# Kernel tuning notes

Measured on AMD Instinct MI355X. Metric: run time of the kernel, lower is better.

## Reference

```python
import jax, jax.numpy as jnp
import numpy as np

B, S, D = 32, 512, 512
H, DH = 8, 64          # head_num, att_embedding_size
DFF = 4 * D
NEG = float(-2**32 + 1)
LN_EPS = 1e-3          # keras LayerNormalization default


def layer_norm(x, gamma, beta):
    mu = jnp.mean(x, axis=-1, keepdims=True)
    var = jnp.mean(jnp.square(x - mu), axis=-1, keepdims=True)
    return (x - mu) / jnp.sqrt(var + LN_EPS) * gamma + beta


def setup_inputs() -> dict:
    key = jax.random.key(0)
    ks = jax.random.split(key, 10)
    queries = jax.random.normal(ks[0], (B, S, D), dtype=jnp.float32)
    keys = jax.random.normal(ks[1], (B, S, D), dtype=jnp.float32)
    query_lens = jax.random.randint(ks[2], (B, 1), 1, S + 1)
    key_lens = jax.random.randint(ks[3], (B, 1), 1, S + 1)
    # learned params (TruncatedNormal stddev 0.05-ish / Glorot approximated by scaled normals)
    W_Q = jax.random.normal(ks[4], (D, D), dtype=jnp.float32) * 0.05
    W_K = jax.random.normal(ks[5], (D, D), dtype=jnp.float32) * 0.05
    W_V = jax.random.normal(ks[6], (D, D), dtype=jnp.float32) * 0.05
    fw1 = jax.random.normal(ks[7], (D, DFF), dtype=jnp.float32) * (1.0 / np.sqrt(D))
    fw2 = jax.random.normal(ks[8], (DFF, D), dtype=jnp.float32) * (1.0 / np.sqrt(DFF))
    ln_gamma = jnp.ones((D,), dtype=jnp.float32)
    ln_beta = jnp.zeros((D,), dtype=jnp.float32)
    return {"queries": queries, "keys": keys, "W_Q": W_Q, "W_K": W_K, "W_V": W_V,
            "fw1": fw1, "fw2": fw2, "ln_gamma": ln_gamma, "ln_beta": ln_beta,
            "query_lens": query_lens, "key_lens": key_lens}


def reference(queries, keys, W_Q, W_K, W_V, fw1, fw2, ln_gamma, ln_beta, query_lens, key_lens):
    # masks from sequence lengths: [B, S] float {0,1}
    pos = jnp.arange(S)
    q_mask = (pos[None, :] < query_lens).astype(queries.dtype)  # [B,S]
    k_mask = (pos[None, :] < key_lens).astype(queries.dtype)    # [B,S]

    # QKV projections, split into heads: [B,S,H,DH]
    Q = (queries @ W_Q).reshape(B, S, H, DH)
    Kp = (keys @ W_K).reshape(B, S, H, DH)
    V = (keys @ W_V).reshape(B, S, H, DH)

    # scaled dot-product scores: [B,H,Sq,Sk]
    scores = jnp.einsum('bqhd,bkhd->bhqk', Q, Kp) / jnp.sqrt(jnp.asarray(DH, queries.dtype))

    # key padding mask
    scores = jnp.where(k_mask[:, None, None, :] == 1, scores, NEG)
    # blinding: kill the diagonal (self-position)
    eye = jnp.eye(S, dtype=bool)
    scores = jnp.where(eye[None, None, :, :], NEG, scores)

    scores = scores - jnp.max(scores, axis=-1, keepdims=True)
    attn = jax.nn.softmax(scores, axis=-1)
    # query mask zeros out padded query rows (after softmax, as in source)
    attn = attn * q_mask[:, None, :, None]

    out = jnp.einsum('bhqk,bkhd->bqhd', attn, V).reshape(B, S, D)

    result = out + queries                       # use_res
    result = layer_norm(result, ln_gamma, ln_beta)  # shared ln (use_layer_norm)

    # feed-forward
    h = jax.nn.relu(result @ fw1) @ fw2
    result = result + h
    result = layer_norm(result, ln_gamma, ln_beta)

    # output_type == 'mean'
    return jnp.mean(result, axis=1, keepdims=True)  # [B,1,D]
```

## Files before the change

kernel.cpp:

```cpp
#include <hip/hip_runtime.h>

typedef unsigned short ushort_t;
typedef unsigned int uint_t;
typedef __attribute__((ext_vector_type(4))) float f32x4;
typedef __attribute__((ext_vector_type(2))) float f32x2;
typedef __attribute__((ext_vector_type(8))) short s16x8;
typedef __attribute__((ext_vector_type(8))) _Float16 f16x8;
typedef __attribute__((ext_vector_type(4))) unsigned short u16x4;

#define NEGV -60000.0f

__device__ __forceinline__ ushort_t f2bf(float f) {
  unsigned int u = __builtin_bit_cast(unsigned int, f);
  return (ushort_t)((u + 0x7fffu + ((u >> 16) & 1u)) >> 16);
}
__device__ __forceinline__ float bf2f(ushort_t h) {
  unsigned int u = ((unsigned int)h) << 16;
  return __builtin_bit_cast(float, u);
}
__device__ __forceinline__ void gload_lds16(const void* g, void* l) {
  __builtin_amdgcn_global_load_lds(
      (const __attribute__((address_space(1))) unsigned int*)g,
      (__attribute__((address_space(3))) unsigned int*)l, 16, 0, 0);
}

template<int EPI>
__global__ __launch_bounds__(512, 2)
void gemm256(const ushort_t* __restrict__ A, const ushort_t* __restrict__ A2,
             int lda,
             const ushort_t* __restrict__ Bt, int ldb,
             void* __restrict__ Cv, int ldc, int K,
             long long sB, long long sC)
{
  __shared__ ushort_t Asm[2][16384];
  __shared__ ushort_t Bsm[2][16384];

  const int tid = threadIdx.x, wid = tid >> 6, lane = tid & 63;
  const int wr = wid >> 2, wc = wid & 3;
  const int fr = lane & 15, fq = lane >> 4;
  const int z = blockIdx.z;

  const ushort_t* Az = (z == 0) ? A : A2;
  const ushort_t* Bz = Bt + (size_t)z * sB;

  const int orig = blockIdx.x + gridDim.x * blockIdx.y;
  const int bx = (orig >> 3) % gridDim.x;
  const int by = (orig & 7) + 8 * ((orig >> 3) / gridDim.x);
  const int m0 = by * 256, n0 = bx * 256;

  const int rr0 = tid >> 3;
  const int ks = (((tid & 7) ^ (rr0 & 7)) * 8);

  auto stageA = [&](int p, int kt, int h) {
    const ushort_t* s = Az + (size_t)(m0 + h * 128 + rr0) * lda + kt * 64 + ks;
    ushort_t* d = &Asm[p][h * 8192 + tid * 8];
    gload_lds16(s, d);
    gload_lds16(s + (size_t)64 * lda, d + 4096);
  };
  auto stageB = [&](int p, int kt, int h) {
    const ushort_t* s = Bz + (size_t)(n0 + h * 128 + rr0) * ldb + kt * 64 + ks;
    ushort_t* d = &Bsm[p][h * 8192 + tid * 8];
    gload_lds16(s, d);
    gload_lds16(s + (size_t)64 * ldb, d + 4096);
  };
  auto ldA = [&](int p, int mi, int kc) -> s16x8 {
    const int R = wr * 128 + mi * 16 + fr;
    return *(const s16x8*)(&Asm[p][R * 64 + (((kc * 4 + fq) ^ (fr & 7)) * 8)]);
  };
  auto ldB = [&](int p, int ni, int kc) -> s16x8 {
    const int R = wc * 64 + ni * 16 + fr;
    return *(const s16x8*)(&Bsm[p][R * 64 + (((kc * 4 + fq) ^ (fr & 7)) * 8)]);
  };

  f32x4 acc[8][4];
#pragma unroll
  for (int m = 0; m < 8; ++m)
#pragma unroll
    for (int n = 0; n < 4; ++n)
      acc[m][n] = (f32x4){0.f, 0.f, 0.f, 0.f};

  const int nk = K >> 6;
  const int niter = nk >> 1;

  stageB(0, 0, 0); stageB(0, 0, 1);
  stageA(0, 0, 0); stageA(0, 0, 1);
  stageB(1, 1, 0); stageB(1, 1, 1);
  asm volatile("s_waitcnt vmcnt(4)" ::: "memory");
  __builtin_amdgcn_s_barrier();

  s16x8 af[4][2], bf[4][2];

  for (int it = 0; it < niter; ++it) {
    const int T = 2 * it;
    const bool more = (it + 1 < niter);

#pragma unroll
    for (int mi = 0; mi < 4; ++mi)
#pragma unroll
      for (int kc = 0; kc < 2; ++kc) af[mi][kc] = ldA(0, mi, kc);
#pragma unroll
    for (int ni = 0; ni < 2; ++ni)
#pragma unroll
      for (int kc = 0; kc < 2; ++kc) bf[ni][kc] = ldB(0, ni, kc);
    stageA(1, T + 1, 0);
    __builtin_amdgcn_s_barrier();
    asm volatile("s_waitcnt lgkmcnt(0)" ::: "memory");
    __builtin_amdgcn_s_setprio(1);
#pragma unroll
    for (int mi = 0; mi < 4; ++mi)
#pragma unroll
      for (int ni = 0; ni < 2; ++ni)
#pragma unroll
        for (int kc = 0; kc < 2; ++kc)
          acc[mi][ni] = __builtin_amdgcn_mfma_f32_16x16x32_bf16(
              af[mi][kc], bf[ni][kc], acc[mi][ni], 0, 0, 0);
    __builtin_amdgcn_s_setprio(0);
    __builtin_amdgcn_s_barrier();

#pragma unroll
    for (int ni = 2; ni < 4; ++ni)
#pragma unroll
      for (int kc = 0; kc < 2; ++kc) bf[ni][kc] = ldB(0, ni, kc);
    stageA(1, T + 1, 1);
    __builtin_amdgcn_s_barrier();
    asm volatile("s_waitcnt lgkmcnt(0)" ::: "memory");
    __builtin_amdgcn_s_setprio(1);
#pragma unroll
    for (int mi = 0; mi < 4; ++mi)
#pragma unroll
      for (int ni = 2; ni < 4; ++ni)
#pragma unroll
        for (int kc = 0; kc < 2; ++kc)
          acc[mi][ni] = __builtin_amdgcn_mfma_f32_16x16x32_bf16(
              af[mi][kc], bf[ni][kc], acc[mi][ni], 0, 0, 0);
    __builtin_amdgcn_s_setprio(0);
    __builtin_amdgcn_s_barrier();

#pragma unroll
    for (int mi = 0; mi < 4; ++mi)
#pragma unroll
      for (int kc = 0; kc < 2; ++kc) af[mi][kc] = ldA(0, 4 + mi, kc);
    if (more) stageB(0, T + 2, 0);
    __builtin_amdgcn_s_barrier();
    asm volatile("s_waitcnt lgkmcnt(0)" ::: "memory");
    __builtin_amdgcn_s_setprio(1);
#pragma unroll
    for (int mi = 0; mi < 4; ++mi)
#pragma unroll
      for (int ni = 0; ni < 2; ++ni)
#pragma unroll
        for (int kc = 0; kc < 2; ++kc)
          acc[4 + mi][ni] = __builtin_amdgcn_mfma_f32_16x16x32_bf16(
              af[mi][kc], bf[ni][kc], acc[4 + mi][ni], 0, 0, 0);
    __builtin_amdgcn_s_setprio(0);
    __builtin_amdgcn_s_barrier();

    if (more) {
      stageB(0, T + 2, 1);
      asm volatile("s_waitcnt vmcnt(4)" ::: "memory");
    } else {
      asm volatile("s_waitcnt vmcnt(0)" ::: "memory");
    }
    __builtin_amdgcn_s_barrier();
    __builtin_amdgcn_s_setprio(1);
#pragma unroll
    for (int mi = 0; mi < 4; ++mi)
#pragma unroll
      for (int ni = 2; ni < 4; ++ni)
#pragma unroll
        for (int kc = 0; kc < 2; ++kc)
          acc[4 + mi][ni] = __builtin_amdgcn_mfma_f32_16x16x32_bf16(
              af[mi][kc], bf[ni][kc], acc[4 + mi][ni], 0, 0, 0);
    __builtin_amdgcn_s_setprio(0);
    __builtin_amdgcn_s_barrier();

#pragma unroll
    for (int mi = 0; mi < 4; ++mi)
#pragma unroll
      for (int kc = 0; kc < 2; ++kc) af[mi][kc] = ldA(1, mi, kc);
#pragma unroll
    for (int ni = 0; ni < 2; ++ni)
#pragma unroll
      for (int kc = 0; kc < 2; ++kc) bf[ni][kc] = ldB(1, ni, kc);
    if (more) stageA(0, T + 2, 0);
    __builtin_amdgcn_s_barrier();
    asm volatile("s_waitcnt lgkmcnt(0)" ::: "memory");
    __builtin_amdgcn_s_setprio(1);
#pragma unroll
    for (int mi = 0; mi < 4; ++mi)
#pragma unroll
      for (int ni = 0; ni < 2; ++ni)
#pragma unroll
        for (int kc = 0; kc < 2; ++kc)
          acc[mi][ni] = __builtin_amdgcn_mfma_f32_16x16x32_bf16(
              af[mi][kc], bf[ni][kc], acc[mi][ni], 0, 0, 0);
    __builtin_amdgcn_s_setprio(0);
    __builtin_amdgcn_s_barrier();

#pragma unroll
    for (int ni = 2; ni < 4; ++ni)
#pragma unroll
      for (int kc = 0; kc < 2; ++kc) bf[ni][kc] = ldB(1, ni, kc);
    if (more) stageA(0, T + 2, 1);
    __builtin_amdgcn_s_barrier();
    asm volatile("s_waitcnt lgkmcnt(0)" ::: "memory");
    __builtin_amdgcn_s_setprio(1);
#pragma unroll
    for (int mi = 0; mi < 4; ++mi)
#pragma unroll
      for (int ni = 2; ni < 4; ++ni)
#pragma unroll
        for (int kc = 0; kc < 2; ++kc)
          acc[mi][ni] = __builtin_amdgcn_mfma_f32_16x16x32_bf16(
              af[mi][kc], bf[ni][kc], acc[mi][ni], 0, 0, 0);
    __builtin_amdgcn_s_setprio(0);
    __builtin_amdgcn_s_barrier();

#pragma unroll
    for (int mi = 0; mi < 4; ++mi)
#pragma unroll
      for (int kc = 0; kc < 2; ++kc) af[mi][kc] = ldA(1, 4 + mi, kc);
    if (more) stageB(1, T + 3, 0);
    __builtin_amdgcn_s_barrier();
    asm volatile("s_waitcnt lgkmcnt(0)" ::: "memory");
    __builtin_amdgcn_s_setprio(1);
#pragma unroll
    for (int mi = 0; mi < 4; ++mi)
#pragma unroll
      for (int ni = 0; ni < 2; ++ni)
#pragma unroll
        for (int kc = 0; kc < 2; ++kc)
          acc[4 + mi][ni] = __builtin_amdgcn_mfma_f32_16x16x32_bf16(
              af[mi][kc], bf[ni][kc], acc[4 + mi][ni], 0, 0, 0);
    __builtin_amdgcn_s_setprio(0);
    __builtin_amdgcn_s_barrier();

    if (more) {
      stageB(1, T + 3, 1);
      asm volatile("s_waitcnt vmcnt(4)" ::: "memory");
    } else {
      asm volatile("s_waitcnt vmcnt(0)" ::: "memory");
    }
    __builtin_amdgcn_s_barrier();
    __builtin_amdgcn_s_setprio(1);
#pragma unroll
    for (int mi = 0; mi < 4; ++mi)
#pragma unroll
      for (int ni = 2; ni < 4; ++ni)
#pragma unroll
        for (int kc = 0; kc < 2; ++kc)
          acc[4 + mi][ni] = __builtin_amdgcn_mfma_f32_16x16x32_bf16(
              af[mi][kc], bf[ni][kc], acc[4 + mi][ni], 0, 0, 0);
    __builtin_amdgcn_s_setprio(0);
    __builtin_amdgcn_s_barrier();
  }

  const float s0 = (EPI == 4 && z == 0) ? 0.125f : 1.0f;
  char* Cz = (char*)Cv + (size_t)sC * z;
  const int rb = fq * 4;
#pragma unroll
  for (int mi = 0; mi < 8; ++mi)
#pragma unroll
    for (int ni = 0; ni < 4; ++ni)
#pragma unroll
      for (int j = 0; j < 4; ++j) {
        const int rg = m0 + wr * 128 + mi * 16 + rb + j;
        const int cg = n0 + wc * 64 + ni * 16 + fr;
        float v = acc[mi][ni][j];
        const size_t idx = (size_t)rg * ldc + cg;
        if constexpr (EPI == 0) {
          ((float*)Cz)[idx] = v;
        } else if constexpr (EPI == 2) {
          ((ushort_t*)Cz)[idx] = f2bf(fmaxf(v, 0.f));
        } else {
          ((ushort_t*)Cz)[idx] = f2bf(v * s0);
        }
      }
}

__global__ __launch_bounds__(256, 4)
void flash_attn(const ushort_t* __restrict__ Qg, const ushort_t* __restrict__ Kg,
                const ushort_t* __restrict__ Vt, ushort_t* __restrict__ AOb,
                const int* __restrict__ qlen, const int* __restrict__ klen)
{
  __shared__ ushort_t sm[20480];
  ushort_t* PQ = sm + 16384;

  const int tid = threadIdx.x, w = tid >> 6, lane = tid & 63;
  const int fr = lane & 15, fq = lane >> 4;

  int id = blockIdx.x;
  id = (id & 7) * 256 + (id >> 3);
  const int qt = id & 7, h = (id >> 3) & 7, b = id >> 6;
  const int q0 = qt * 64;
  const int KL = klen[b], QL = qlen[b];

  if (q0 >= QL) {
#pragma unroll
    for (int i = 0; i < 4; ++i) {
      int idx = i * 256 + tid;
      int rr = idx >> 4, cc = (idx & 15) << 2;
      *(u16x4*)&AOb[((size_t)(b * 512 + q0 + rr)) * 512 + h * 64 + cc] =
          (u16x4){0, 0, 0, 0};
    }
    return;
  }

  int nt = (KL + 63) >> 6;
  if (KL == 1) nt = 8;

  const ushort_t* Qrow = Qg + ((size_t)(b * 512 + q0)) * 512 + h * 64;
  const ushort_t* Krow = Kg + ((size_t)b * 512) * 512 + h * 64;
  const ushort_t* Vrow = Vt + (((size_t)b * 8 + h) * 64) * 512;

#pragma unroll
  for (int i = 0; i < 2; ++i) {
    int s = i * 256 + tid, r = s >> 3, c = (s & 7) ^ (r & 7);
    gload_lds16(Qrow + (size_t)r * 512 + c * 8, PQ + (i * 256 + w * 64) * 8);
  }
#pragma unroll
  for (int i = 0; i < 2; ++i) {
    int s = i * 256 + tid, r = s >> 3, c = (s & 7) ^ (r & 7);
    gload_lds16(Krow + (size_t)r * 512 + c * 8, sm + (i * 256 + w * 64) * 8);
    gload_lds16(Vrow + (size_t)r * 512 + c * 8, sm + 4096 + (i * 256 + w * 64) * 8);
  }
  __syncthreads();

  s16x8 qf[2];
#pragma unroll
  for (int kc = 0; kc < 2; ++kc) {
    int r = w * 16 + fr;
    qf[kc] = *(const s16x8*)(PQ + r * 64 + (((kc * 4 + fq) ^ (r & 7)) * 8));
  }

  float mrun[4], lrun[4];
  f32x4 oacc[4];
#pragma unroll
  for (int j = 0; j < 4; ++j) { mrun[j] = -1e30f; lrun[j] = 0.f; }
#pragma unroll
  for (int nd = 0; nd < 4; ++nd) oacc[nd] = (f32x4){0.f, 0.f, 0.f, 0.f};

  for (int t = 0; t < nt; ++t) {
    ushort_t* Kb = sm + (t & 1) * 8192;
    ushort_t* Vb = Kb + 4096;
    if (t + 1 < nt) {
      const int kv1 = (t + 1) * 64;
      ushort_t* Kn = sm + ((t + 1) & 1) * 8192;
#pragma unroll
      for (int i = 0; i < 2; ++i) {
        int s = i * 256 + tid, r = s >> 3, c = (s & 7) ^ (r & 7);
        gload_lds16(Krow + (size_t)(kv1 + r) * 512 + c * 8,
                    Kn + (i * 256 + w * 64) * 8);
        gload_lds16(Vrow + (size_t)r * 512 + kv1 + c * 8,
                    Kn + 4096 + (i * 256 + w * 64) * 8);
      }
    }
    const int kv0 = t * 64;

    f32x4 sacc[4];
#pragma unroll
    for (int n = 0; n < 4; ++n) sacc[n] = (f32x4){0.f, 0.f, 0.f, 0.f};
#pragma unroll
    for (int n = 0; n < 4; ++n)
#pragma unroll
      for (int kc = 0; kc < 2; ++kc) {
        int r = n * 16 + fr;
        s16x8 kf = *(const s16x8*)(Kb + r * 64 + (((kc * 4 + fq) ^ (r & 7)) * 8));
        sacc[n] = __builtin_amdgcn_mfma_f32_16x16x32_bf16(qf[kc], kf, sacc[n], 0, 0, 0);
      }

#pragma unroll
    for (int j = 0; j < 4; ++j) {
      const int rl = w * 16 + fq * 4 + j;
      const int rg = q0 + rl;
      float sv[4];
      float tmax = -1e30f;
#pragma unroll
      for (int n = 0; n < 4; ++n) {
        int cg = kv0 + n * 16 + fr;
        float v = sacc[n][j];
        if (cg >= KL || cg == rg) v = NEGV;
        sv[n] = v;
        tmax = fmaxf(tmax, v);
      }
#pragma unroll
      for (int o = 1; o < 16; o <<= 1) tmax = fmaxf(tmax, __shfl_xor(tmax, o));
      const float mnew = fmaxf(mrun[j], tmax);
      const float sf = __expf(mrun[j] - mnew);
      mrun[j] = mnew;
      float ps = 0.f;
      _Float16* prow = (_Float16*)(PQ + rl * 64);
#pragma unroll
      for (int n = 0; n < 4; ++n) {
        float p = __expf(sv[n] - mnew);
        ps += p;
        int cl = n * 2 + (fr >> 3);
        prow[((cl ^ (rl & 7)) * 8) + (fr & 7)] = (_Float16)p;
      }
      lrun[j] = lrun[j] * sf + ps;
#pragma unroll
      for (int nd = 0; nd < 4; ++nd) oacc[nd][j] *= sf;
    }

#pragma unroll
    for (int kc = 0; kc < 2; ++kc) {
      const int rl = w * 16 + fr;
      s16x8 pf = *(const s16x8*)(PQ + rl * 64 + (((kc * 4 + fq) ^ (rl & 7)) * 8));
#pragma unroll
      for (int nd = 0; nd < 4; ++nd) {
        int d = nd * 16 + fr;
        s16x8 vf = *(const s16x8*)(Vb + d * 64 + (((kc * 4 + fq) ^ (d & 7)) * 8));
        oacc[nd] = __builtin_amdgcn_mfma_f32_16x16x32_f16(
            __builtin_bit_cast(f16x8, pf), __builtin_bit_cast(f16x8, vf),
            oacc[nd], 0, 0, 0);
      }
    }
    __syncthreads();
  }

#pragma unroll
  for (int j = 0; j < 4; ++j) {
    float l = lrun[j];
#pragma unroll
    for (int o = 1; o < 16; o <<= 1) l += __shfl_xor(l, o);
    const int rg = q0 + w * 16 + fq * 4 + j;
    const float inv = (rg < QL) ? (1.f / l) : 0.f;
#pragma unroll
    for (int nd = 0; nd < 4; ++nd)
      AOb[((size_t)(b * 512 + rg)) * 512 + h * 64 + nd * 16 + fr] =
          f2bf(oacc[nd][j] * inv);
  }
}

__global__ __launch_bounds__(256) void cvt_bf16(const float* __restrict__ in,
                                                ushort_t* __restrict__ out, int n4) {
  int i = blockIdx.x * 256 + threadIdx.x;
  if (i >= n4) return;
  f32x4 v = ((const f32x4*)in)[i];
  u16x4 o;
#pragma unroll
  for (int j = 0; j < 4; ++j) o[j] = f2bf(v[j]);
  ((u16x4*)out)[i] = o;
}

__global__ __launch_bounds__(256) void transpose_cvt(const float* __restrict__ in,
                                                     ushort_t* __restrict__ out,
                                                     int R, int C) {
  __shared__ float tile[32][33];
  const int c0 = blockIdx.x * 32, r0 = blockIdx.y * 32;
  const int tx = threadIdx.x & 31, ty = threadIdx.x >> 5;
#pragma unroll
  for (int i = 0; i < 32; i += 8)
    tile[ty + i][tx] = in[(size_t)(r0 + ty + i) * C + (c0 + tx)];
  __syncthreads();
#pragma unroll
  for (int i = 0; i < 32; i += 8)
    out[(size_t)(c0 + ty + i) * R + (r0 + tx)] = f2bf(tile[tx][ty + i]);
}

__global__ __launch_bounds__(256) void build_vt(const ushort_t* __restrict__ V,
                                                ushort_t* __restrict__ Vt) {
  __shared__ ushort_t tile[64 * 65];
  const int s0 = blockIdx.x * 64, h = blockIdx.y, b = blockIdx.z;
  const int t = threadIdx.x;
#pragma unroll
  for (int i = 0; i < 16; ++i) {
    int idx = i * 256 + t;
    int sl = idx >> 6, d = idx & 63;
    tile[sl * 65 + d] = V[(size_t)(b * 512 + s0 + sl) * 512 + h * 64 + d];
  }
  __syncthreads();
  _Float16* vt = (_Float16*)Vt;
#pragma unroll
  for (int i = 0; i < 16; ++i) {
    int idx = i * 256 + t;
    int d = idx >> 6, sl = idx & 63;
    vt[((size_t)(b * 8 + h) * 64 + d) * 512 + (s0 + sl)] =
        (_Float16)bf2f(tile[sl * 65 + d]);
  }
}

__global__ __launch_bounds__(256) void ln1(const ushort_t* __restrict__ xb,
                                           const float* __restrict__ r,
                                           const float* __restrict__ g,
                                           const float* __restrict__ be,
                                           ushort_t* __restrict__ ob) {
  const int row = blockIdx.x, t = threadIdx.x;
  const size_t base = (size_t)row * 512;
  const uint_t xv = ((const uint_t*)(xb + base))[t];
  const f32x2 rv = ((const f32x2*)(r + base))[t];
  float v0 = bf2f((ushort_t)(xv & 0xffff)) + rv[0];
  float v1 = bf2f((ushort_t)(xv >> 16)) + rv[1];
  float s = v0 + v1, q = v0 * v0 + v1 * v1;
#pragma unroll
  for (int o = 32; o; o >>= 1) { s += __shfl_xor(s, o); q += __shfl_xor(q, o); }
  __shared__ float ps[4], pq[4];
  const int w = t >> 6, lane = t & 63;
  if (lane == 0) { ps[w] = s; pq[w] = q; }
  __syncthreads();
  s = ps[0] + ps[1] + ps[2] + ps[3];
  q = pq[0] + pq[1] + pq[2] + pq[3];
  const float mu = s * 0.001953125f;
  const float var = q * 0.001953125f - mu * mu;
  const float inv = 1.0f / sqrtf(var + 1e-3f);
  const float y0 = (v0 - mu) * inv * g[2 * t] + be[2 * t];
  const float y1 = (v1 - mu) * inv * g[2 * t + 1] + be[2 * t + 1];
  ((uint_t*)(ob + base))[t] = (uint_t)f2bf(y0) | ((uint_t)f2bf(y1) << 16);
}

__global__ __launch_bounds__(256) void ln2(const float* __restrict__ h2a,
                                           const float* __restrict__ h2b,
                                           const ushort_t* __restrict__ r1b,
                                           const float* __restrict__ g,
                                           const float* __restrict__ be,
                                           ushort_t* __restrict__ ob) {
  const int row = blockIdx.x, t = threadIdx.x;
  const size_t base = (size_t)row * 512;
  const f32x2 a = ((const f32x2*)(h2a + base))[t];
  const f32x2 b = ((const f32x2*)(h2b + base))[t];
  const uint_t rv = ((const uint_t*)(r1b + base))[t];
  float v0 = a[0] + b[0] + bf2f((ushort_t)(rv & 0xffff));
  float v1 = a[1] + b[1] + bf2f((ushort_t)(rv >> 16));
  float s = v0 + v1, q = v0 * v0 + v1 * v1;
#pragma unroll
  for (int o = 32; o; o >>= 1) { s += __shfl_xor(s, o); q += __shfl_xor(q, o); }
  __shared__ float ps[4], pq[4];
  const int w = t >> 6, lane = t & 63;
  if (lane == 0) { ps[w] = s; pq[w] = q; }
  __syncthreads();
  s = ps[0] + ps[1] + ps[2] + ps[3];
  q = pq[0] + pq[1] + pq[2] + pq[3];
  const float mu = s * 0.001953125f;
  const float var = q * 0.001953125f - mu * mu;
  const float inv = 1.0f / sqrtf(var + 1e-3f);
  const float y0 = (v0 - mu) * inv * g[2 * t] + be[2 * t];
  const float y1 = (v1 - mu) * inv * g[2 * t + 1] + be[2 * t + 1];
  ((uint_t*)(ob + base))[t] = (uint_t)f2bf(y0) | ((uint_t)f2bf(y1) << 16);
}

__global__ void mean_partial(const ushort_t* __restrict__ r3,
                             float* __restrict__ part) {
  const int sc = blockIdx.x, b = blockIdx.y, d = threadIdx.x;
  float s = 0.f;
#pragma unroll 4
  for (int i = 0; i < 64; ++i)
    s += bf2f(r3[(size_t)(b * 512 + sc * 64 + i) * 512 + d]);
  part[(size_t)(b * 8 + sc) * 512 + d] = s;
}
__global__ void mean_final(const float* __restrict__ part, float* __restrict__ out) {
  const int b = blockIdx.x, d = threadIdx.x;
  float s = 0.f;
#pragma unroll
  for (int i = 0; i < 8; ++i) s += part[(size_t)(b * 8 + i) * 512 + d];
  out[b * 512 + d] = s * (1.0f / 512.0f);
}

extern "C" void kernel_launch(void* const* d_in, const int* in_sizes, int n_in,
                              void* d_out, int out_size, void* d_ws, size_t ws_size,
                              hipStream_t stream) {
  (void)in_sizes; (void)n_in; (void)out_size; (void)ws_size;
  const float* queries = (const float*)d_in[0];
  const float* keys    = (const float*)d_in[1];
  const float* W_Q = (const float*)d_in[2];
  const float* W_K = (const float*)d_in[3];
  const float* W_V = (const float*)d_in[4];
  const float* fw1 = (const float*)d_in[5];
  const float* fw2 = (const float*)d_in[6];
  const float* ln_g = (const float*)d_in[7];
  const float* ln_b = (const float*)d_in[8];
  const int* qlen = (const int*)d_in[9];
  const int* klen = (const int*)d_in[10];
  float* out = (float*)d_out;

  char* ws = (char*)d_ws;
  const size_t MB = 1048576;
  ushort_t* XQ  = (ushort_t*)(ws + 0 * MB);
  ushort_t* XK  = (ushort_t*)(ws + 16 * MB);
  ushort_t* Qb  = (ushort_t*)(ws + 32 * MB);
  ushort_t* Vb  = (ushort_t*)(ws + 64 * MB);
  ushort_t* VT  = (ushort_t*)(ws + 80 * MB);
  ushort_t* AOb = (ushort_t*)(ws + 96 * MB);
  ushort_t* R1B = (ushort_t*)(ws + 112 * MB);
  ushort_t* H1  = (ushort_t*)(ws + 0 * MB);
  float*    H2  = (float*)(ws + 128 * MB);
  ushort_t* R3B = (ushort_t*)(ws + 192 * MB);
  char*     wsw = ws + 208 * MB;
  ushort_t* WQT  = (ushort_t*)(wsw);
  ushort_t* FW1T = (ushort_t*)(wsw + 3 * 524288);
  ushort_t* FW2T = (ushort_t*)(wsw + 3 * 524288 + 2097152);
  float*    PART = (float*)(wsw + 3 * 524288 + 2 * 2097152);

  cvt_bf16<<<8192, 256, 0, stream>>>(queries, XQ, 2097152);
  cvt_bf16<<<8192, 256, 0, stream>>>(keys, XK, 2097152);
  transpose_cvt<<<dim3(16, 16), 256, 0, stream>>>(W_Q, WQT, 512, 512);
  transpose_cvt<<<dim3(16, 16), 256, 0, stream>>>(W_K, WQT + 262144, 512, 512);
  transpose_cvt<<<dim3(16, 16), 256, 0, stream>>>(W_V, WQT + 524288, 512, 512);
  transpose_cvt<<<dim3(64, 16), 256, 0, stream>>>(fw1, FW1T, 512, 2048);
  transpose_cvt<<<dim3(16, 64), 256, 0, stream>>>(fw2, FW2T, 2048, 512);
  gemm256<4><<<dim3(2, 64, 3), 512, 0, stream>>>(
      XQ, XK, 512, WQT, 512, (void*)Qb, 512, 512, 262144, 16 * MB);
  build_vt<<<dim3(8, 8, 32), 256, 0, stream>>>(Vb, VT);
  flash_attn<<<2048, 256, 0, stream>>>(Qb, Qb + 8388608, VT, AOb, qlen, klen);
  ln1<<<16384, 256, 0, stream>>>(AOb, queries, ln_g, ln_b, R1B);
  gemm256<2><<<dim3(8, 64, 1), 512, 0, stream>>>(
      R1B, R1B, 512, FW1T, 512, (void*)H1, 2048, 512, 0, 0);
  gemm256<0><<<dim3(2, 64, 2), 512, 0, stream>>>(
      H1, H1 + 1024, 2048, FW2T, 2048, (void*)H2, 512, 1024, 1024, 32 * MB);
  ln2<<<16384, 256, 0, stream>>>(H2, H2 + 8388608, R1B, ln_g, ln_b, R3B);
  mean_partial<<<dim3(8, 32), 512, 0, stream>>>(R3B, PART);
  mean_final<<<32, 512, 0, stream>>>(PART, out);
}
```

Baseline: 247.3 us.

## Restructure GEMM main loop into four phases and merge prep kernels

The GEMM inner loop drops from eight half-width MFMA phases with a barrier each to four full-width phases. Whole A/B half-tiles are now staged in pairs with adjusted vmcnt waits, and the prologue also prefetches A for the second k-step. Separately, the seven bf16 conversion and transpose launches are merged into one prep kernel that dispatches on block index. The aim is to cut barrier and launch overhead, at the cost of more live B fragments in registers and coarser overlap of memory loads with MFMA work.

```diff
diff --git a/kernel.cpp b/kernel.cpp
--- a/kernel.cpp
+++ b/kernel.cpp
@@ -84,8 +84,9 @@
 
   stageB(0, 0, 0); stageB(0, 0, 1);
   stageA(0, 0, 0); stageA(0, 0, 1);
+  stageA(1, 1, 0); stageA(1, 1, 1);
   stageB(1, 1, 0); stageB(1, 1, 1);
-  asm volatile("s_waitcnt vmcnt(4)" ::: "memory");
+  asm volatile("s_waitcnt vmcnt(8)" ::: "memory");
   __builtin_amdgcn_s_barrier();
 
   s16x8 af[4][2], bf[4][2];
@@ -99,17 +100,17 @@
 #pragma unroll
       for (int kc = 0; kc < 2; ++kc) af[mi][kc] = ldA(0, mi, kc);
 #pragma unroll
-    for (int ni = 0; ni < 2; ++ni)
+    for (int ni = 0; ni < 4; ++ni)
 #pragma unroll
       for (int kc = 0; kc < 2; ++kc) bf[ni][kc] = ldB(0, ni, kc);
-    stageA(1, T + 1, 0);
+    if (it) { stageA(1, T + 1, 0); stageA(1, T + 1, 1); }
     __builtin_amdgcn_s_barrier();
     asm volatile("s_waitcnt lgkmcnt(0)" ::: "memory");
     __builtin_amdgcn_s_setprio(1);
 #pragma unroll
     for (int mi = 0; mi < 4; ++mi)
 #pragma unroll
-      for (int ni = 0; ni < 2; ++ni)
+      for (int ni = 0; ni < 4; ++ni)
 #pragma unroll
         for (int kc = 0; kc < 2; ++kc)
           acc[mi][ni] = __builtin_amdgcn_mfma_f32_16x16x32_bf16(
@@ -118,17 +119,45 @@
     __builtin_amdgcn_s_barrier();
 
 #pragma unroll
-    for (int ni = 2; ni < 4; ++ni)
-#pragma unroll
-      for (int kc = 0; kc < 2; ++kc) bf[ni][kc] = ldB(0, ni, kc);
-    stageA(1, T + 1, 1);
+    for (int mi = 0; mi < 4; ++mi)
+#pragma unroll
+      for (int kc = 0; kc < 2; ++kc) af[mi][kc] = ldA(0, 4 + mi, kc);
+    if (more) {
+      stageB(0, T + 2, 0); stageB(0, T + 2, 1);
+      asm volatile("s_waitcnt vmcnt(4)" ::: "memory");
+    } else {
+      asm volatile("s_waitcnt vmcnt(0)" ::: "memory");
+    }
     __builtin_amdgcn_s_barrier();
     asm volatile("s_waitcnt lgkmcnt(0)" ::: "memory");
     __builtin_amdgcn_s_setprio(1);
 #pragma unroll
     for (int mi = 0; mi < 4; ++mi)
 #pragma unroll
-      for (int ni = 2; ni < 4; ++ni)
+      for (int ni = 0; ni < 4; ++ni)
+#pragma unroll
+        for (int kc = 0; kc < 2; ++kc)
+          acc[4 + mi][ni] = __builtin_amdgcn_mfma_f32_16x16x32_bf16(
+              af[mi][kc], bf[ni][kc], acc[4 + mi][ni], 0, 0, 0);
+    __builtin_amdgcn_s_setprio(0);
+    __builtin_amdgcn_s_barrier();
+
+#pragma unroll
+    for (int mi = 0; mi < 4; ++mi)
+#pragma unroll
+      for (int kc = 0; kc < 2; ++kc) af[mi][kc] = ldA(1, mi, kc);
+#pragma unroll
+    for (int ni = 0; ni < 4; ++ni)
+#pragma unroll
+      for (int kc = 0; kc < 2; ++kc) bf[ni][kc] = ldB(1, ni, kc);
+    if (more) { stageA(0, T + 2, 0); stageA(0, T + 2, 1); }
+    __builtin_amdgcn_s_barrier();
+    asm volatile("s_waitcnt lgkmcnt(0)" ::: "memory");
+    __builtin_amdgcn_s_setprio(1);
+#pragma unroll
+    for (int mi = 0; mi < 4; ++mi)
+#pragma unroll
+      for (int ni = 0; ni < 4; ++ni)
 #pragma unroll
         for (int kc = 0; kc < 2; ++kc)
           acc[mi][ni] = __builtin_amdgcn_mfma_f32_16x16x32_bf16(
@@ -139,114 +168,20 @@
 #pragma unroll
     for (int mi = 0; mi < 4; ++mi)
 #pragma unroll
-      for (int kc = 0; kc < 2; ++kc) af[mi][kc] = ldA(0, 4 + mi, kc);
-    if (more) stageB(0, T + 2, 0);
-    __builtin_amdgcn_s_barrier();
-    asm volatile("s_waitcnt lgkmcnt(0)" ::: "memory");
-    __builtin_amdgcn_s_setprio(1);
-#pragma unroll
-    for (int mi = 0; mi < 4; ++mi)
-#pragma unroll
-      for (int ni = 0; ni < 2; ++ni)
-#pragma unroll
-        for (int kc = 0; kc < 2; ++kc)
-          acc[4 + mi][ni] = __builtin_amdgcn_mfma_f32_16x16x32_bf16(
-              af[mi][kc], bf[ni][kc], acc[4 + mi][ni], 0, 0, 0);
-    __builtin_amdgcn_s_setprio(0);
-    __builtin_amdgcn_s_barrier();
-
+      for (int kc = 0; kc < 2; ++kc) af[mi][kc] = ldA(1, 4 + mi, kc);
     if (more) {
-      stageB(0, T + 2, 1);
+      stageB(1, T + 3, 0); stageB(1, T + 3, 1);
       asm volatile("s_waitcnt vmcnt(4)" ::: "memory");
     } else {
       asm volatile("s_waitcnt vmcnt(0)" ::: "memory");
     }
     __builtin_amdgcn_s_barrier();
-    __builtin_amdgcn_s_setprio(1);
-#pragma unroll
-    for (int mi = 0; mi < 4; ++mi)
-#pragma unroll
-      for (int ni = 2; ni < 4; ++ni)
-#pragma unroll
-        for (int kc = 0; kc < 2; ++kc)
-          acc[4 + mi][ni] = __builtin_amdgcn_mfma_f32_16x16x32_bf16(
-              af[mi][kc], bf[ni][kc], acc[4 + mi][ni], 0, 0, 0);
-    __builtin_amdgcn_s_setprio(0);
-    __builtin_amdgcn_s_barrier();
-
-#pragma unroll
-    for (int mi = 0; mi < 4; ++mi)
-#pragma unroll
-      for (int kc = 0; kc < 2; ++kc) af[mi][kc] = ldA(1, mi, kc);
-#pragma unroll
-    for (int ni = 0; ni < 2; ++ni)
-#pragma unroll
-      for (int kc = 0; kc < 2; ++kc) bf[ni][kc] = ldB(1, ni, kc);
-    if (more) stageA(0, T + 2, 0);
-    __builtin_amdgcn_s_barrier();
     asm volatile("s_waitcnt lgkmcnt(0)" ::: "memory");
     __builtin_amdgcn_s_setprio(1);
 #pragma unroll
     for (int mi = 0; mi < 4; ++mi)
 #pragma unroll
-      for (int ni = 0; ni < 2; ++ni)
-#pragma unroll
-        for (int kc = 0; kc < 2; ++kc)
-          acc[mi][ni] = __builtin_amdgcn_mfma_f32_16x16x32_bf16(
-              af[mi][kc], bf[ni][kc], acc[mi][ni], 0, 0, 0);
-    __builtin_amdgcn_s_setprio(0);
-    __builtin_amdgcn_s_barrier();
-
-#pragma unroll
-    for (int ni = 2; ni < 4; ++ni)
-#pragma unroll
-      for (int kc = 0; kc < 2; ++kc) bf[ni][kc] = ldB(1, ni, kc);
-    if (more) stageA(0, T + 2, 1);
-    __builtin_amdgcn_s_barrier();
-    asm volatile("s_waitcnt lgkmcnt(0)" ::: "memory");
-    __builtin_amdgcn_s_setprio(1);
-#pragma unroll
-    for (int mi = 0; mi < 4; ++mi)
-#pragma unroll
-      for (int ni = 2; ni < 4; ++ni)
-#pragma unroll
-        for (int kc = 0; kc < 2; ++kc)
-          acc[mi][ni] = __builtin_amdgcn_mfma_f32_16x16x32_bf16(
-              af[mi][kc], bf[ni][kc], acc[mi][ni], 0, 0, 0);
-    __builtin_amdgcn_s_setprio(0);
-    __builtin_amdgcn_s_barrier();
-
-#pragma unroll
-    for (int mi = 0; mi < 4; ++mi)
-#pragma unroll
-      for (int kc = 0; kc < 2; ++kc) af[mi][kc] = ldA(1, 4 + mi, kc);
-    if (more) stageB(1, T + 3, 0);
-    __builtin_amdgcn_s_barrier();
-    asm volatile("s_waitcnt lgkmcnt(0)" ::: "memory");
-    __builtin_amdgcn_s_setprio(1);
-#pragma unroll
-    for (int mi = 0; mi < 4; ++mi)
-#pragma unroll
-      for (int ni = 0; ni < 2; ++ni)
-#pragma unroll
-        for (int kc = 0; kc < 2; ++kc)
-          acc[4 + mi][ni] = __builtin_amdgcn_mfma_f32_16x16x32_bf16(
-              af[mi][kc], bf[ni][kc], acc[4 + mi][ni], 0, 0, 0);
-    __builtin_amdgcn_s_setprio(0);
-    __builtin_amdgcn_s_barrier();
-
-    if (more) {
-      stageB(1, T + 3, 1);
-      asm volatile("s_waitcnt vmcnt(4)" ::: "memory");
-    } else {
-      asm volatile("s_waitcnt vmcnt(0)" ::: "memory");
-    }
-    __builtin_amdgcn_s_barrier();
-    __builtin_amdgcn_s_setprio(1);
-#pragma unroll
-    for (int mi = 0; mi < 4; ++mi)
-#pragma unroll
-      for (int ni = 2; ni < 4; ++ni)
+      for (int ni = 0; ni < 4; ++ni)
 #pragma unroll
         for (int kc = 0; kc < 2; ++kc)
           acc[4 + mi][ni] = __builtin_amdgcn_mfma_f32_16x16x32_bf16(
@@ -278,6 +213,55 @@
       }
 }
 
+__global__ __launch_bounds__(256)
+void prep(const float* __restrict__ q, const float* __restrict__ k,
+          ushort_t* __restrict__ XQ, ushort_t* __restrict__ XK,
+          const float* __restrict__ W_Q, const float* __restrict__ W_K,
+          const float* __restrict__ W_V,
+          const float* __restrict__ fw1, const float* __restrict__ fw2,
+          ushort_t* __restrict__ WQT, ushort_t* __restrict__ FW1T,
+          ushort_t* __restrict__ FW2T)
+{
+  __shared__ float tile[32][33];
+  int bid = blockIdx.x;
+  if (bid < 16384) {
+    const float* in = (bid < 8192) ? q : k;
+    ushort_t* outp = (bid < 8192) ? XQ : XK;
+    int i = (bid & 8191) * 256 + threadIdx.x;
+    f32x4 v = ((const f32x4*)in)[i];
+    u16x4 o;
+#pragma unroll
+    for (int j = 0; j < 4; ++j) o[j] = f2bf(v[j]);
+    ((u16x4*)outp)[i] = o;
+    return;
+  }
+  bid -= 16384;
+  const float* in;
+  ushort_t* outp;
+  int R, C, bx, by;
+  if (bid < 768) {
+    int zz = bid >> 8, idx = bid & 255;
+    in = (zz == 0) ? W_Q : (zz == 1) ? W_K : W_V;
+    outp = WQT + zz * 262144;
+    R = 512; C = 512; bx = idx & 15; by = idx >> 4;
+  } else if (bid < 1792) {
+    int idx = bid - 768;
+    in = fw1; outp = FW1T; R = 512; C = 2048; bx = idx & 63; by = idx >> 6;
+  } else {
+    int idx = bid - 1792;
+    in = fw2; outp = FW2T; R = 2048; C = 512; bx = idx & 15; by = idx >> 4;
+  }
+  const int c0 = bx * 32, r0 = by * 32;
+  const int tx = threadIdx.x & 31, ty = threadIdx.x >> 5;
+#pragma unroll
+  for (int i = 0; i < 32; i += 8)
+    tile[ty + i][tx] = in[(size_t)(r0 + ty + i) * C + (c0 + tx)];
+  __syncthreads();
+#pragma unroll
+  for (int i = 0; i < 32; i += 8)
+    outp[(size_t)(c0 + ty + i) * R + (r0 + tx)] = f2bf(tile[tx][ty + i]);
+}
+
 __global__ __launch_bounds__(256, 4)
 void flash_attn(const ushort_t* __restrict__ Qg, const ushort_t* __restrict__ Kg,
                 const ushort_t* __restrict__ Vt, ushort_t* __restrict__ AOb,
@@ -430,32 +414,6 @@
       AOb[((size_t)(b * 512 + rg)) * 512 + h * 64 + nd * 16 + fr] =
           f2bf(oacc[nd][j] * inv);
   }
-}
-
-__global__ __launch_bounds__(256) void cvt_bf16(const float* __restrict__ in,
-                                                ushort_t* __restrict__ out, int n4) {
-  int i = blockIdx.x * 256 + threadIdx.x;
-  if (i >= n4) return;
-  f32x4 v = ((const f32x4*)in)[i];
-  u16x4 o;
-#pragma unroll
-  for (int j = 0; j < 4; ++j) o[j] = f2bf(v[j]);
-  ((u16x4*)out)[i] = o;
-}
-
-__global__ __launch_bounds__(256) void transpose_cvt(const float* __restrict__ in,
-                                                     ushort_t* __restrict__ out,
-                                                     int R, int C) {
-  __shared__ float tile[32][33];
-  const int c0 = blockIdx.x * 32, r0 = blockIdx.y * 32;
-  const int tx = threadIdx.x & 31, ty = threadIdx.x >> 5;
-#pragma unroll
-  for (int i = 0; i < 32; i += 8)
-    tile[ty + i][tx] = in[(size_t)(r0 + ty + i) * C + (c0 + tx)];
-  __syncthreads();
-#pragma unroll
-  for (int i = 0; i < 32; i += 8)
-    out[(size_t)(c0 + ty + i) * R + (r0 + tx)] = f2bf(tile[tx][ty + i]);
 }
 
 __global__ __launch_bounds__(256) void build_vt(const ushort_t* __restrict__ V,
@@ -590,13 +548,8 @@
   ushort_t* FW2T = (ushort_t*)(wsw + 3 * 524288 + 2097152);
   float*    PART = (float*)(wsw + 3 * 524288 + 2 * 2097152);
 
-  cvt_bf16<<<8192, 256, 0, stream>>>(queries, XQ, 2097152);
-  cvt_bf16<<<8192, 256, 0, stream>>>(keys, XK, 2097152);
-  transpose_cvt<<<dim3(16, 16), 256, 0, stream>>>(W_Q, WQT, 512, 512);
-  transpose_cvt<<<dim3(16, 16), 256, 0, stream>>>(W_K, WQT + 262144, 512, 512);
-  transpose_cvt<<<dim3(16, 16), 256, 0, stream>>>(W_V, WQT + 524288, 512, 512);
-  transpose_cvt<<<dim3(64, 16), 256, 0, stream>>>(fw1, FW1T, 512, 2048);
-  transpose_cvt<<<dim3(16, 64), 256, 0, stream>>>(fw2, FW2T, 2048, 512);
+  prep<<<19200, 256, 0, stream>>>(queries, keys, XQ, XK, W_Q, W_K, W_V,
+                                  fw1, fw2, WQT, FW1T, FW2T);
   gemm256<4><<<dim3(2, 64, 3), 512, 0, stream>>>(
       XQ, XK, 512, WQT, 512, (void*)Qb, 512, 512, 262144, 16 * MB);
   build_vt<<<dim3(8, 8, 32), 256, 0, stream>>>(Vb, VT);
```

Measured after the change: 233.6 us. -5.5%, faster.
